# Kernel tuning notes

Hardware: AMD Instinct MI355X
Metric: run time of the kernel (lower is better)

The kernel has to match this reference:

```python
import jax, jax.numpy as jnp
import numpy as np

NUM_HEADS = 8

def _gelu(x):
    return jax.nn.gelu(x, approximate=False)

def _ln(x, w, b, eps=1e-5):
    m = x.mean(-1, keepdims=True)
    v = ((x - m) ** 2).mean(-1, keepdims=True)
    return (x - m) / jnp.sqrt(v + eps) * w + b

def _conv(x, w, pad):
    return jax.lax.conv_general_dilated(x, w, (1, 1), [(pad, pad), (pad, pad)],
                                        dimension_numbers=('NCHW', 'OIHW', 'NCHW'))

def _dwconv(x, w):
    return jax.lax.conv_general_dilated(x, w, (1, 1), [(1, 1), (1, 1)],
                                        feature_group_count=x.shape[1],
                                        dimension_numbers=('NCHW', 'OIHW', 'NCHW'))

def setup_inputs():
    B, T, N, C, K = 4, 3, 4096, 256, 100
    ks = jax.random.split(jax.random.key(0), 16)
    p = lambda i, shape: (0.02 * jax.random.normal(ks[i], shape)).astype(jnp.float32)
    z = lambda n: jnp.zeros((n,), jnp.float32)
    return {
        'x': jax.random.normal(ks[0], (B, N, C), jnp.float32),
        'mem': jax.random.normal(ks[1], (B * T, N, C), jnp.float32),
        'conv1_w': p(2, (C, C, 7, 7)), 'conv1_b': z(C),
        'conv2_w': p(3, (C, C, 1, 1)), 'conv2_b': z(C),
        'conv3_w': p(4, (K, C, 1, 1)),
        'sim_alpha': jnp.ones((1,), jnp.float32), 'sim_beta': jnp.zeros((1,), jnp.float32),
        'ln_w': jnp.ones((C,), jnp.float32), 'ln_b': z(C),
        'q_w': p(5, (C, C)), 'q_b': z(C),
        'k_w': p(6, (C, C)), 'k_b': z(C),
        'v_w': p(7, (C, C)), 'v_b': z(C),
        'proj_w': p(8, (C, C)), 'proj_b': z(C),
        'fc1_w': p(9, (4 * C, C)), 'fc1_b': z(4 * C),
        'dw_w': p(10, (4 * C, 1, 3, 3)), 'dw_b': z(4 * C),
        'fc2_w': p(11, (C, 4 * C)), 'fc2_b': z(C),
        'H': 64, 'W': 64, 't': 3,
    }

def reference(x, mem, conv1_w, conv1_b, conv2_w, conv2_b, conv3_w, sim_alpha, sim_beta,
              ln_w, ln_b, q_w, q_b, k_w, k_b, v_w, v_b, proj_w, proj_b,
              fc1_w, fc1_b, dw_w, dw_b, fc2_w, fc2_b, H, W, t):
    B, N, C = x.shape
    T = t + 1
    # stack memory frames with current frame: [B, T, N, C]
    xt = jnp.concatenate([mem.reshape(B, t, N, C), x[:, None]], axis=1)
    img = xt.reshape(B * T, N, C).transpose(0, 2, 1).reshape(B * T, C, H, W)
    h = _gelu(_conv(img, conv1_w, 3) + conv1_b[:, None, None])
    h = _gelu(_conv(h, conv2_w, 0) + conv2_b[:, None, None])
    cz = _conv(h, conv3_w, 0)                      # [B*T, K, H, W]
    K = cz.shape[1]
    center = jax.nn.softmax(cz.reshape(B, T, K, N), axis=-1)
    center = jnp.einsum('btkn,btnc->btkc', center, xt)  # cluster centers [B,T,K,C]
    last, prev = center[:, -1], center[:, :-1]
    num = jnp.einsum('bkc,bskc->bsk', last, prev)
    den = jnp.maximum(jnp.linalg.norm(last, axis=-1)[:, None] * jnp.linalg.norm(prev, axis=-1), 1e-8)
    cos = jax.nn.sigmoid(sim_beta + sim_alpha * (num / den))  # [B, T-1, K]
    C_in = last + (cos[..., None] * prev).sum(axis=1)
    C_in = _ln(C_in, ln_w, ln_b)
    # cross-attention: queries = current frame tokens, keys/values = centers
    hd = C // NUM_HEADS
    q = (x @ q_w.T + q_b).reshape(B, N, NUM_HEADS, hd) * (hd ** -0.5)
    k = (C_in @ k_w.T + k_b).reshape(B, K, NUM_HEADS, hd)
    v = (C_in @ v_w.T + v_b).reshape(B, K, NUM_HEADS, hd)
    attn = jax.nn.softmax(jnp.einsum('bnhd,bkhd->bhnk', q, k), axis=-1)
    o = jnp.einsum('bhnk,bkhd->bnhd', attn, v).reshape(B, N, C)
    o = o @ proj_w.T + proj_b
    out = x + _ln(o, ln_w, ln_b)
    # MLP with depthwise conv
    y = out @ fc1_w.T + fc1_b                      # [B, N, 4C]
    yi = y.transpose(0, 2, 1).reshape(B, 4 * C, H, W)
    yi = _dwconv(yi, dw_w) + dw_b[:, None, None]
    y = _gelu(yi.reshape(B, 4 * C, N).transpose(0, 2, 1))
    y = y @ fc2_w.T + fc2_b
    return out + _ln(y, ln_w, ln_b)
```

## Files before the change

### kernel.cpp

```cpp
#include <hip/hip_runtime.h>
#include <math.h>

#define NN 4096
#define CC 256
#define HH 64
#define BT 16
#define KCC 100
#define NHH 8
#define HDD 32
#define C4 1024

typedef unsigned short bf16_t;
typedef short s16x8 __attribute__((ext_vector_type(8)));
typedef float f32x4 __attribute__((ext_vector_type(4)));

__device__ __forceinline__ float bf2f(bf16_t h) {
  return __uint_as_float(((unsigned)h) << 16);
}
__device__ __forceinline__ bf16_t f2bf(float f) {
  unsigned u = __float_as_uint(f);
  return (bf16_t)((u + 0x7FFFu + ((u >> 16) & 1u)) >> 16);
}

__device__ __forceinline__ float gelu_f(float x) {
  return 0.5f * x * (1.0f + erff(x * 0.7071067811865475f));
}

__device__ __forceinline__ void g2l16(const void* g, void* l) {
  __builtin_amdgcn_global_load_lds((const __attribute__((address_space(1))) void*)g,
                                   (__attribute__((address_space(3))) void*)l, 16, 0, 0);
}

__device__ __forceinline__ float block_sum256(float v) {
  __shared__ float sh[4];
#pragma unroll
  for (int off = 32; off; off >>= 1) v += __shfl_xor(v, off, 64);
  __syncthreads();
  if ((threadIdx.x & 63) == 0) sh[threadIdx.x >> 6] = v;
  __syncthreads();
  return sh[0] + sh[1] + sh[2] + sh[3];
}

__device__ __forceinline__ const float* xt_base(const float* x, const float* mem, int bt) {
  int b = bt >> 2, tt = bt & 3;
  return (tt < 3) ? (mem + (size_t)(b * 3 + tt) * NN * CC)
                  : (x + (size_t)b * NN * CC);
}

__global__ __launch_bounds__(256) void prologue(const float* __restrict__ x,
                                                const float* __restrict__ mem,
                                                bf16_t* __restrict__ xtb,
                                                const float* __restrict__ w1,
                                                bf16_t* __restrict__ wtb,
                                                const float* __restrict__ c2w,
                                                const float* __restrict__ c3w,
                                                const float* __restrict__ qw,
                                                const float* __restrict__ pw,
                                                const float* __restrict__ f1w,
                                                const float* __restrict__ f2w,
                                                bf16_t* __restrict__ wbz) {
  int bid = blockIdx.x;
  int tid = threadIdx.x;
  if (bid < 16384) {
    int i = bid * 256 + tid;
    int c4 = i & 63;
    int n = (i >> 6) & 4095;
    int bt = i >> 18;
    const float* src = xt_base(x, mem, bt) + (size_t)n * CC + c4 * 4;
    float4 v = *(const float4*)src;
    ushort4 o;
    o.x = f2bf(v.x); o.y = f2bf(v.y); o.z = f2bf(v.z); o.w = f2bf(v.w);
    *(ushort4*)(xtb + (size_t)i * 4) = o;
  } else if (bid < 19520) {
    int i = (bid - 16384) * 256 + tid;
    int cj = i & 7;
    int t = i >> 3;
    int co = t & 63; t >>= 6;
    int oc = t & 3; t >>= 2;
    int kx = t % 7; t /= 7;
    int cq = t & 3; t >>= 2;
    int cg = t & 7;
    int ky = t >> 3;
    int ci = cg * 32 + oc * 8 + cj;
    int cog = cq * 64 + co;
    wtb[i] = f2bf(w1[((size_t)(cog * CC + ci) * 7 + ky) * 7 + kx]);
  } else {
    int j = (bid - 19520) * 256 + tid;
    float v;
    if (j < 65536) v = c2w[j];
    else if (j < 91136) v = c3w[j - 65536];
    else if (j < 156672) v = qw[j - 91136];
    else if (j < 222208) v = pw[j - 156672];
    else if (j < 484352) v = f1w[j - 222208];
    else v = f2w[j - 484352];
    wbz[j] = f2bf(v);
  }
}

__global__ __launch_bounds__(256, 2) void conv1_mfma(const bf16_t* __restrict__ xtb,
                                                     const bf16_t* __restrict__ wtb,
                                                     const float* __restrict__ bias,
                                                     bf16_t* __restrict__ h1) {
  int cq = blockIdx.x >> 8;
  int bt = (blockIdx.x >> 4) & 15;
  int h0 = (blockIdx.x & 15) * 4;
  int co0 = cq * 64;
  int tid = threadIdx.x;
  int wv = tid >> 6;
  int lane = tid & 63;
  int lm = lane & 15;
  int g = lane >> 4;
  __shared__ short As[10][4][70][8];
  __shared__ short Ws[7][4][64][8];
  {
    s16x8 z = {0, 0, 0, 0, 0, 0, 0, 0};
    for (int i = tid; i < 2800; i += 256) *(s16x8*)((short*)As + i * 8) = z;
  }
  __syncthreads();
  f32x4 acc[4][4] = {};
  const bf16_t* xb = xtb + (size_t)bt * (NN * CC);
  for (int cig = 0; cig < 8; ++cig) {
    int ci0 = cig * 32;
    for (int t = wv; t < 40; t += 4) {
      int rr = t >> 2, go = t & 3;
      int r = h0 - 3 + rr;
      if (r >= 0 && r < HH) {
        const bf16_t* gsrc = xb + ((size_t)(r * 64 + lane)) * CC + ci0 + go * 8;
        g2l16(gsrc, &As[rr][go][3][0]);
      }
    }
    for (int ky = 0; ky < 7; ++ky) {
      const bf16_t* wk = wtb + ((size_t)((ky * 8 + cig) * 4 + cq)) * (1792 * 8);
      for (int t = wv; t < 28; t += 4)
        g2l16(wk + (size_t)t * 512 + lane * 8, (short*)Ws + t * 512);
      __syncthreads();
#pragma unroll
      for (int kx = 0; kx < 7; ++kx) {
        s16x8 af[4], bf[4];
#pragma unroll
        for (int mt = 0; mt < 4; ++mt)
          af[mt] = *(const s16x8*)&As[wv + ky][g][mt * 16 + lm + kx][0];
#pragma unroll
        for (int nt = 0; nt < 4; ++nt)
          bf[nt] = *(const s16x8*)&Ws[kx][g][nt * 16 + lm][0];
#pragma unroll
        for (int mt = 0; mt < 4; ++mt)
#pragma unroll
          for (int nt = 0; nt < 4; ++nt)
            acc[mt][nt] = __builtin_amdgcn_mfma_f32_16x16x32_bf16(af[mt], bf[nt],
                                                                  acc[mt][nt], 0, 0, 0);
      }
      __syncthreads();
    }
  }
  int row = h0 + wv;
  const size_t xbase = (size_t)bt * (NN * CC);
#pragma unroll
  for (int nt = 0; nt < 4; ++nt) {
    int co = co0 + nt * 16 + lm;
    float bs = bias[co];
#pragma unroll
    for (int mt = 0; mt < 4; ++mt) {
#pragma unroll
      for (int rg = 0; rg < 4; ++rg) {
        int col = mt * 16 + g * 4 + rg;
        float vv = acc[mt][nt][rg] + bs;
        h1[xbase + (size_t)(row * 64 + col) * CC + co] = f2bf(gelu_f(vv));
      }
    }
  }
}

template <int GELU, int BIAS, int TOUT, int OBF>
__global__ __launch_bounds__(256) void gemm_mfma(const bf16_t* __restrict__ A,
                                                 const bf16_t* __restrict__ W,
                                                 const float* __restrict__ bias,
                                                 void* __restrict__ outp,
                                                 int M, int N, int K, int ldo,
                                                 size_t aStr, size_t oStr) {
  __shared__ short As[128][40];
  __shared__ short Bs[128][40];
  A += (size_t)blockIdx.z * aStr;
  size_t obase = (size_t)blockIdx.z * oStr;
  int tid = threadIdx.x;
  int n0 = blockIdx.x * 128, m0 = blockIdx.y * 128;
  int lane = tid & 63, wv = tid >> 6;
  int wm = wv & 1, wn = wv >> 1;
  int lm = lane & 15, g = lane >> 4;
  f32x4 acc[4][4] = {};
  int r1 = tid >> 2, kq = tid & 3;
  int r2 = r1 + 64;
  for (int k0 = 0; k0 < K; k0 += 32) {
    *(s16x8*)&As[r1][kq * 8] = *(const s16x8*)(A + (size_t)(m0 + r1) * K + k0 + kq * 8);
    *(s16x8*)&As[r2][kq * 8] = *(const s16x8*)(A + (size_t)(m0 + r2) * K + k0 + kq * 8);
    s16x8 z = {0, 0, 0, 0, 0, 0, 0, 0};
    s16x8 b1 = z, b2 = z;
    if (n0 + r1 < N) b1 = *(const s16x8*)(W + (size_t)(n0 + r1) * K + k0 + kq * 8);
    if (n0 + r2 < N) b2 = *(const s16x8*)(W + (size_t)(n0 + r2) * K + k0 + kq * 8);
    *(s16x8*)&Bs[r1][kq * 8] = b1;
    *(s16x8*)&Bs[r2][kq * 8] = b2;
    __syncthreads();
    s16x8 af[4], bf[4];
#pragma unroll
    for (int mt = 0; mt < 4; ++mt)
      af[mt] = *(const s16x8*)&As[wm * 64 + mt * 16 + lm][g * 8];
#pragma unroll
    for (int nt = 0; nt < 4; ++nt)
      bf[nt] = *(const s16x8*)&Bs[wn * 64 + nt * 16 + lm][g * 8];
#pragma unroll
    for (int mt = 0; mt < 4; ++mt)
#pragma unroll
      for (int nt = 0; nt < 4; ++nt)
        acc[mt][nt] = __builtin_amdgcn_mfma_f32_16x16x32_bf16(af[mt], bf[nt],
                                                              acc[mt][nt], 0, 0, 0);
    __syncthreads();
  }
#pragma unroll
  for (int nt = 0; nt < 4; ++nt) {
    int n = n0 + wn * 64 + nt * 16 + lm;
    if (n >= N) continue;
    float bs = BIAS ? bias[n] : 0.f;
#pragma unroll
    for (int mt = 0; mt < 4; ++mt) {
#pragma unroll
      for (int rg = 0; rg < 4; ++rg) {
        int m = m0 + wm * 64 + mt * 16 + g * 4 + rg;
        float v = acc[mt][nt][rg] + bs;
        if (GELU) v = gelu_f(v);
        size_t idx = obase + (TOUT ? ((size_t)n * ldo + m) : ((size_t)m * ldo + n));
        if (OBF)
          ((bf16_t*)outp)[idx] = f2bf(v);
        else
          ((float*)outp)[idx] = v;
      }
    }
  }
}

__global__ __launch_bounds__(256) void gemm_kv(const float* __restrict__ cin,
                                               const float* __restrict__ kw,
                                               const float* __restrict__ kbias,
                                               const float* __restrict__ vw,
                                               const float* __restrict__ vbias,
                                               float* __restrict__ kout,
                                               float* __restrict__ vout) {
  const float* Wm = blockIdx.z ? vw : kw;
  const float* bias = blockIdx.z ? vbias : kbias;
  float* outp = blockIdx.z ? vout : kout;
  const int M = 400, N = 256, K = 256;
  __shared__ float As[16][68];
  __shared__ float Ws[16][68];
  int tid = threadIdx.x;
  int n0 = blockIdx.x * 64, m0 = blockIdx.y * 64;
  int txn = tid & 15, tym = tid >> 4;
  int mi = tid >> 2, kq = (tid & 3) * 4;
  float acc[4][4] = {};
  for (int k0 = 0; k0 < K; k0 += 16) {
    float4 av = {0, 0, 0, 0}, wvv = {0, 0, 0, 0};
    if (m0 + mi < M) av = *(const float4*)&cin[(size_t)(m0 + mi) * K + k0 + kq];
    if (n0 + mi < N) wvv = *(const float4*)&Wm[(size_t)(n0 + mi) * K + k0 + kq];
    As[kq + 0][mi] = av.x; As[kq + 1][mi] = av.y; As[kq + 2][mi] = av.z; As[kq + 3][mi] = av.w;
    Ws[kq + 0][mi] = wvv.x; Ws[kq + 1][mi] = wvv.y; Ws[kq + 2][mi] = wvv.z; Ws[kq + 3][mi] = wvv.w;
    __syncthreads();
#pragma unroll
    for (int ki = 0; ki < 16; ++ki) {
      float4 a4 = *(const float4*)&As[ki][tym * 4];
      float4 w4 = *(const float4*)&Ws[ki][txn * 4];
      float am[4] = {a4.x, a4.y, a4.z, a4.w};
      float wn[4] = {w4.x, w4.y, w4.z, w4.w};
#pragma unroll
      for (int i = 0; i < 4; ++i)
#pragma unroll
        for (int j = 0; j < 4; ++j) acc[i][j] += am[i] * wn[j];
    }
    __syncthreads();
  }
#pragma unroll
  for (int i = 0; i < 4; ++i) {
    int m = m0 + tym * 4 + i;
    if (m >= M) continue;
#pragma unroll
    for (int j = 0; j < 4; ++j) {
      int n = n0 + txn * 4 + j;
      outp[(size_t)m * 256 + n] = acc[i][j] + bias[n];
    }
  }
}

__global__ __launch_bounds__(256) void softmax_rows(bf16_t* __restrict__ p) {
  __shared__ float sh[8];
  int tid = threadIdx.x;
  bf16_t* base = p + (size_t)blockIdx.x * NN + tid * 16;
  s16x8 a = *(const s16x8*)base;
  s16x8 b = *(const s16x8*)(base + 8);
  float vals[16];
#pragma unroll
  for (int j = 0; j < 8; ++j) {
    vals[j] = bf2f((bf16_t)a[j]);
    vals[8 + j] = bf2f((bf16_t)b[j]);
  }
  float mx = -1e30f;
#pragma unroll
  for (int j = 0; j < 16; ++j) mx = fmaxf(mx, vals[j]);
#pragma unroll
  for (int off = 32; off; off >>= 1) mx = fmaxf(mx, __shfl_xor(mx, off, 64));
  if ((tid & 63) == 0) sh[tid >> 6] = mx;
  __syncthreads();
  mx = fmaxf(fmaxf(sh[0], sh[1]), fmaxf(sh[2], sh[3]));
  float s = 0.f;
#pragma unroll
  for (int j = 0; j < 16; ++j) {
    vals[j] = expf(vals[j] - mx);
    s += vals[j];
  }
#pragma unroll
  for (int off = 32; off; off >>= 1) s += __shfl_xor(s, off, 64);
  if ((tid & 63) == 0) sh[4 + (tid >> 6)] = s;
  __syncthreads();
  s = sh[4] + sh[5] + sh[6] + sh[7];
  float inv = 1.f / s;
  s16x8 oa, ob;
#pragma unroll
  for (int j = 0; j < 8; ++j) {
    oa[j] = (short)f2bf(vals[j] * inv);
    ob[j] = (short)f2bf(vals[8 + j] * inv);
  }
  *(s16x8*)base = oa;
  *(s16x8*)(base + 8) = ob;
}

__global__ __launch_bounds__(256) void center_mfma(const bf16_t* __restrict__ soft,
                                                   const bf16_t* __restrict__ xtb,
                                                   float* __restrict__ partial) {
  int c0 = blockIdx.x * 128;
  int bt = blockIdx.y;
  int nc = blockIdx.z;
  int tid = threadIdx.x;
  int lane = tid & 63, wv = tid >> 6;
  int wm = wv & 1, wn = wv >> 1;
  int lm = lane & 15, g = lane >> 4;
  __shared__ short As[128][40];
  __shared__ short Bs[128][40];
  f32x4 acc[4][4] = {};
  int r1 = tid >> 2, kq = tid & 3;
  int r2 = r1 + 64;
  int bk = tid & 31, bc = (tid >> 5) * 16;
  const bf16_t* sb = soft + (size_t)bt * NN + (size_t)nc * 512;
  const bf16_t* xb = xtb + ((size_t)bt * NN + (size_t)nc * 512) * CC + c0;
  for (int k0 = 0; k0 < 512; k0 += 32) {
    *(s16x8*)&As[r1][kq * 8] =
        *(const s16x8*)(sb + (size_t)r1 * (BT * NN) + k0 + kq * 8);
    if (r2 < KCC)
      *(s16x8*)&As[r2][kq * 8] =
          *(const s16x8*)(sb + (size_t)r2 * (BT * NN) + k0 + kq * 8);
    s16x8 v0 = *(const s16x8*)(xb + (size_t)(k0 + bk) * CC + bc);
    s16x8 v1 = *(const s16x8*)(xb + (size_t)(k0 + bk) * CC + bc + 8);
#pragma unroll
    for (int j = 0; j < 8; ++j) Bs[bc + j][bk] = v0[j];
#pragma unroll
    for (int j = 0; j < 8; ++j) Bs[bc + 8 + j][bk] = v1[j];
    __syncthreads();
    s16x8 af[4], bf[4];
#pragma unroll
    for (int mt = 0; mt < 4; ++mt)
      af[mt] = *(const s16x8*)&As[wm * 64 + mt * 16 + lm][g * 8];
#pragma unroll
    for (int nt = 0; nt < 4; ++nt)
      bf[nt] = *(const s16x8*)&Bs[wn * 64 + nt * 16 + lm][g * 8];
#pragma unroll
    for (int mt = 0; mt < 4; ++mt)
#pragma unroll
      for (int nt = 0; nt < 4; ++nt)
        acc[mt][nt] = __builtin_amdgcn_mfma_f32_16x16x32_bf16(af[mt], bf[nt],
                                                              acc[mt][nt], 0, 0, 0);
    __syncthreads();
  }
  size_t obase = ((size_t)nc * BT + bt) * (KCC * CC);
#pragma unroll
  for (int nt = 0; nt < 4; ++nt) {
    int c = c0 + wn * 64 + nt * 16 + lm;
#pragma unroll
    for (int mt = 0; mt < 4; ++mt) {
#pragma unroll
      for (int rg = 0; rg < 4; ++rg) {
        int m = wm * 64 + mt * 16 + g * 4 + rg;
        if (m < KCC) partial[obase + (size_t)m * CC + c] = acc[mt][nt][rg];
      }
    }
  }
}

__global__ __launch_bounds__(256) void sim_cin(const float* __restrict__ partial,
                                               const float* __restrict__ alpha_p,
                                               const float* __restrict__ beta_p,
                                               const float* __restrict__ lnw,
                                               const float* __restrict__ lnb,
                                               float* __restrict__ cin) {
  int b = blockIdx.x / KCC, kc = blockIdx.x % KCC;
  int c = threadIdx.x;
  float p0 = 0.f, p1 = 0.f, p2 = 0.f, lst = 0.f;
#pragma unroll
  for (int nc = 0; nc < 8; ++nc) {
    size_t base = ((size_t)nc * BT) * KCC * CC;
    p0 += partial[base + ((size_t)(b * 4 + 0) * KCC + kc) * CC + c];
    p1 += partial[base + ((size_t)(b * 4 + 1) * KCC + kc) * CC + c];
    p2 += partial[base + ((size_t)(b * 4 + 2) * KCC + kc) * CC + c];
    lst += partial[base + ((size_t)(b * 4 + 3) * KCC + kc) * CC + c];
  }
  float ll = block_sum256(lst * lst);
  float q0 = block_sum256(p0 * p0);
  float q1 = block_sum256(p1 * p1);
  float q2 = block_sum256(p2 * p2);
  float d0 = block_sum256(lst * p0);
  float d1 = block_sum256(lst * p1);
  float d2 = block_sum256(lst * p2);
  float alpha = alpha_p[0], beta = beta_p[0];
  float nl = sqrtf(ll);
  float c0 = 1.f / (1.f + expf(-(beta + alpha * (d0 / fmaxf(nl * sqrtf(q0), 1e-8f)))));
  float c1 = 1.f / (1.f + expf(-(beta + alpha * (d1 / fmaxf(nl * sqrtf(q1), 1e-8f)))));
  float c2 = 1.f / (1.f + expf(-(beta + alpha * (d2 / fmaxf(nl * sqrtf(q2), 1e-8f)))));
  float v = lst + c0 * p0 + c1 * p1 + c2 * p2;
  float m = block_sum256(v) * (1.f / CC);
  float dv = v - m;
  float var = block_sum256(dv * dv) * (1.f / CC);
  cin[((size_t)b * KCC + kc) * CC + c] = dv * rsqrtf(var + 1e-5f) * lnw[c] + lnb[c];
}

__global__ __launch_bounds__(256) void attn2(const float* __restrict__ q,
                                             const float* __restrict__ kb,
                                             const float* __restrict__ vb,
                                             bf16_t* __restrict__ ob) {
  int b = blockIdx.y;
  int n0 = blockIdx.x * 8;
  int tid = threadIdx.x;
  __shared__ float qs[8][256];
  __shared__ float Ks[32][257];
  __shared__ float sc[8][8][104];
#pragma unroll
  for (int r = 0; r < 8; ++r)
    qs[r][tid] = q[((size_t)b * NN + n0 + r) * CC + tid] * 0.17677669529663687f;
  int nn = tid >> 5, kcl = tid & 31;
  for (int kt = 0; kt < 4; ++kt) {
    int kbase = kt * 32;
    int rows = (kbase + 32 <= KCC) ? 32 : (KCC - kbase);
    __syncthreads();
    for (int idx = tid; idx < rows * 256; idx += 256) {
      int rr = idx >> 8, cc = idx & 255;
      Ks[rr][cc] = kb[((size_t)b * KCC + kbase + rr) * CC + cc];
    }
    __syncthreads();
    if (kcl < rows) {
#pragma unroll
      for (int h = 0; h < NHH; ++h) {
        float s = 0.f;
#pragma unroll
        for (int d = 0; d < HDD; ++d) s += qs[nn][h * HDD + d] * Ks[kcl][h * HDD + d];
        sc[nn][h][kbase + kcl] = s;
      }
    }
  }
  __syncthreads();
  {
    int tnn = tid >> 5, th = (tid >> 2) & 7, j = tid & 3;
    float mx = -1e30f;
    for (int kc = j * 25; kc < j * 25 + 25; ++kc) mx = fmaxf(mx, sc[tnn][th][kc]);
    mx = fmaxf(mx, __shfl_xor(mx, 1, 64));
    mx = fmaxf(mx, __shfl_xor(mx, 2, 64));
    float sm = 0.f;
    for (int kc = j * 25; kc < j * 25 + 25; ++kc) {
      float e = expf(sc[tnn][th][kc] - mx);
      sc[tnn][th][kc] = e;
      sm += e;
    }
    sm += __shfl_xor(sm, 1, 64);
    sm += __shfl_xor(sm, 2, 64);
    float inv = 1.f / sm;
    for (int kc = j * 25; kc < j * 25 + 25; ++kc) sc[tnn][th][kc] *= inv;
  }
  __syncthreads();
  float o[8] = {0, 0, 0, 0, 0, 0, 0, 0};
  int h = tid >> 5;
  for (int kc = 0; kc < KCC; ++kc) {
    float v = vb[((size_t)b * KCC + kc) * CC + tid];
#pragma unroll
    for (int r = 0; r < 8; ++r) o[r] += sc[r][h][kc] * v;
  }
#pragma unroll
  for (int r = 0; r < 8; ++r)
    ob[((size_t)b * NN + n0 + r) * CC + tid] = f2bf(o[r]);
}

template <int WB>
__global__ __launch_bounds__(256) void add_ln(const float* __restrict__ res,
                                              const float* __restrict__ y,
                                              const float* __restrict__ lnw,
                                              const float* __restrict__ lnb,
                                              float* __restrict__ dst,
                                              bf16_t* __restrict__ dst_b) {
  size_t row = blockIdx.x;
  int c = threadIdx.x;
  float v = y[row * CC + c];
  float m = block_sum256(v) * (1.f / CC);
  float dv = v - m;
  float var = block_sum256(dv * dv) * (1.f / CC);
  float o = res[row * CC + c] + dv * rsqrtf(var + 1e-5f) * lnw[c] + lnb[c];
  dst[row * CC + c] = o;
  if (WB) dst_b[row * CC + c] = f2bf(o);
}

__global__ __launch_bounds__(256) void dwconv_kernel(const bf16_t* __restrict__ y1,
                                                     const float* __restrict__ dww,
                                                     const float* __restrict__ dwb,
                                                     bf16_t* __restrict__ y2) {
  int b = blockIdx.x >> 12;
  int n = blockIdx.x & 4095;
  int h = n >> 6, w = n & 63;
  int c40 = threadIdx.x * 4;
  float wreg[4][9];
#pragma unroll
  for (int j = 0; j < 4; ++j)
#pragma unroll
    for (int t2 = 0; t2 < 9; ++t2) wreg[j][t2] = dww[(size_t)(c40 + j) * 9 + t2];
  float acc[4] = {0, 0, 0, 0};
#pragma unroll
  for (int dy = 0; dy < 3; ++dy) {
    int r = h + dy - 1;
    if (r < 0 || r >= HH) continue;
#pragma unroll
    for (int dx = 0; dx < 3; ++dx) {
      int cl = w + dx - 1;
      if (cl < 0 || cl >= 64) continue;
      ushort4 u = *(const ushort4*)(y1 + ((size_t)b * NN + r * 64 + cl) * C4 + c40);
      int t2 = dy * 3 + dx;
      acc[0] += bf2f(u.x) * wreg[0][t2];
      acc[1] += bf2f(u.y) * wreg[1][t2];
      acc[2] += bf2f(u.z) * wreg[2][t2];
      acc[3] += bf2f(u.w) * wreg[3][t2];
    }
  }
  ushort4 o;
  o.x = f2bf(gelu_f(acc[0] + dwb[c40 + 0]));
  o.y = f2bf(gelu_f(acc[1] + dwb[c40 + 1]));
  o.z = f2bf(gelu_f(acc[2] + dwb[c40 + 2]));
  o.w = f2bf(gelu_f(acc[3] + dwb[c40 + 3]));
  *(ushort4*)(y2 + ((size_t)b * NN + n) * C4 + c40) = o;
}

extern "C" void kernel_launch(void* const* d_in, const int* in_sizes, int n_in,
                              void* d_out, int out_size, void* d_ws, size_t ws_size,
                              hipStream_t stream) {
  const float* x = (const float*)d_in[0];
  const float* mem = (const float*)d_in[1];
  const float* conv1_w = (const float*)d_in[2];
  const float* conv1_b = (const float*)d_in[3];
  const float* conv2_w = (const float*)d_in[4];
  const float* conv2_b = (const float*)d_in[5];
  const float* conv3_w = (const float*)d_in[6];
  const float* sim_a = (const float*)d_in[7];
  const float* sim_b = (const float*)d_in[8];
  const float* ln_w = (const float*)d_in[9];
  const float* ln_b = (const float*)d_in[10];
  const float* q_w = (const float*)d_in[11];
  const float* q_b = (const float*)d_in[12];
  const float* k_w = (const float*)d_in[13];
  const float* k_b = (const float*)d_in[14];
  const float* v_w = (const float*)d_in[15];
  const float* v_b = (const float*)d_in[16];
  const float* proj_w = (const float*)d_in[17];
  const float* proj_b = (const float*)d_in[18];
  const float* fc1_w = (const float*)d_in[19];
  const float* fc1_b = (const float*)d_in[20];
  const float* dw_w = (const float*)d_in[21];
  const float* dw_b = (const float*)d_in[22];
  const float* fc2_w = (const float*)d_in[23];
  const float* fc2_b = (const float*)d_in[24];

  char* base = (char*)d_ws;
  bf16_t* xtb = (bf16_t*)(base);
  bf16_t* by1 = (bf16_t*)(base);
  bf16_t* bh1 = (bf16_t*)(base + 33554432);
  float* qb = (float*)(base + 33554432);
  float* outb = (float*)(base + 33554432);
  float* partial = (float*)(base + 50331648);
  float* pbuf = (float*)(base + 50331648);
  bf16_t* y2 = (bf16_t*)(base + 50331648);
  bf16_t* czt = (bf16_t*)(base + 67108864);
  bf16_t* obz = (bf16_t*)(base + 67108864);
  bf16_t* outb_b = (bf16_t*)(base + 67108864);
  bf16_t* wtb = (bf16_t*)(base + 80216064);
  bf16_t* h2c = (bf16_t*)(base + 80216064);
  bf16_t* wbz = (bf16_t*)(base + 96993280);
  float* cin = (float*)(base + 100124672);
  float* kb = (float*)(base + 100534272);
  float* vb = (float*)(base + 100943872);
  float* dout = (float*)d_out;

  bf16_t* conv2_wb = wbz;
  bf16_t* conv3_wb = wbz + 65536;
  bf16_t* q_wb = wbz + 91136;
  bf16_t* proj_wb = wbz + 156672;
  bf16_t* fc1_wb = wbz + 222208;
  bf16_t* fc2_wb = wbz + 484352;

  prologue<<<22436, 256, 0, stream>>>(x, mem, xtb, conv1_w, wtb, conv2_w, conv3_w,
                                      q_w, proj_w, fc1_w, fc2_w, wbz);
  conv1_mfma<<<1024, 256, 0, stream>>>(xtb, wtb, conv1_b, bh1);
  for (int i = 0; i < 2; ++i) {
    gemm_mfma<1, 1, 0, 1><<<dim3(2, 256, 1), 256, 0, stream>>>(
        bh1 + (size_t)i * 32768 * CC, conv2_wb, conv2_b, h2c, 32768, 256, 256, 256, 0, 0);
    gemm_mfma<0, 0, 1, 1><<<dim3(1, 256, 1), 256, 0, stream>>>(
        h2c, conv3_wb, nullptr, czt + (size_t)i * 32768, 32768, 100, 256, 65536, 0, 0);
  }
  softmax_rows<<<1600, 256, 0, stream>>>(czt);
  center_mfma<<<dim3(2, 16, 8), 256, 0, stream>>>(czt, xtb, partial);
  sim_cin<<<400, 256, 0, stream>>>(partial, sim_a, sim_b, ln_w, ln_b, cin);
  gemm_mfma<0, 1, 0, 0><<<dim3(2, 32, 4), 256, 0, stream>>>(
      xtb + (size_t)3 * NN * CC, q_wb, q_b, qb, 4096, 256, 256, 256,
      (size_t)4 * NN * CC, (size_t)NN * CC);
  gemm_kv<<<dim3(4, 7, 2), 256, 0, stream>>>(cin, k_w, k_b, v_w, v_b, kb, vb);
  attn2<<<dim3(512, 4), 256, 0, stream>>>(qb, kb, vb, obz);
  gemm_mfma<0, 1, 0, 0><<<dim3(2, 128, 1), 256, 0, stream>>>(obz, proj_wb, proj_b, pbuf,
                                                             16384, 256, 256, 256, 0, 0);
  add_ln<1><<<16384, 256, 0, stream>>>(x, pbuf, ln_w, ln_b, outb, outb_b);
  gemm_mfma<0, 1, 0, 1><<<dim3(8, 128, 1), 256, 0, stream>>>(outb_b, fc1_wb, fc1_b, by1,
                                                             16384, 1024, 256, 1024, 0, 0);
  dwconv_kernel<<<16384, 256, 0, stream>>>(by1, dw_w, dw_b, y2);
  gemm_mfma<0, 1, 0, 0><<<dim3(2, 32, 4), 256, 0, stream>>>(
      y2, fc2_wb, fc2_b, dout, 4096, 256, 1024, 256,
      (size_t)NN * C4, (size_t)NN * CC);
  add_ln<0><<<16384, 256, 0, stream>>>(outb, dout, ln_w, ln_b, dout, nullptr);
}
```

Measured before the change: 895.8 us.

## Enlarge conv1 tile to 16 rows and double-buffer weight loads

The 7x7 conv kernel now processes 16 output rows per block with 512 threads (8 waves, each computing 2 rows) instead of 4 rows with 256 threads. The input halo overhead per block shrinks and each weight tile is reused across more pixels. Weight tiles are double-buffered so the next ky slice loads while the current one is consumed, removing one barrier per step. The cost is twice the accumulator registers per thread, much larger LDS use, and only 256 blocks, which can hurt occupancy and GPU fill.

Result: faster. 868.0 us (-3.1%).

```diff
diff --git a/kernel.cpp b/kernel.cpp
--- a/kernel.cpp
+++ b/kernel.cpp
@@ -97,54 +97,65 @@
   }
 }
 
-__global__ __launch_bounds__(256, 2) void conv1_mfma(const bf16_t* __restrict__ xtb,
+__global__ __launch_bounds__(512, 2) void conv1_mfma(const bf16_t* __restrict__ xtb,
                                                      const bf16_t* __restrict__ wtb,
                                                      const float* __restrict__ bias,
                                                      bf16_t* __restrict__ h1) {
-  int cq = blockIdx.x >> 8;
-  int bt = (blockIdx.x >> 4) & 15;
-  int h0 = (blockIdx.x & 15) * 4;
+  int bid = blockIdx.x;
+  int cq = bid & 3;
+  int rem = bid >> 2;
+  int bt = rem & 15;
+  int rb = rem >> 4;
+  int r0 = rb * 16;
   int co0 = cq * 64;
   int tid = threadIdx.x;
   int wv = tid >> 6;
   int lane = tid & 63;
   int lm = lane & 15;
   int g = lane >> 4;
-  __shared__ short As[10][4][70][8];
-  __shared__ short Ws[7][4][64][8];
+  __shared__ __align__(16) short As[22][4][70][8];
+  __shared__ __align__(16) short Ws[2][7][4][64][8];
   {
     s16x8 z = {0, 0, 0, 0, 0, 0, 0, 0};
-    for (int i = tid; i < 2800; i += 256) *(s16x8*)((short*)As + i * 8) = z;
+    for (int i = tid; i < 22 * 4 * 70; i += 512) *(s16x8*)((short*)As + i * 8) = z;
   }
   __syncthreads();
-  f32x4 acc[4][4] = {};
+  f32x4 acc[8][4] = {};
   const bf16_t* xb = xtb + (size_t)bt * (NN * CC);
   for (int cig = 0; cig < 8; ++cig) {
     int ci0 = cig * 32;
-    for (int t = wv; t < 40; t += 4) {
+    for (int t = wv; t < 88; t += 8) {
       int rr = t >> 2, go = t & 3;
-      int r = h0 - 3 + rr;
+      int r = r0 - 3 + rr;
       if (r >= 0 && r < HH) {
         const bf16_t* gsrc = xb + ((size_t)(r * 64 + lane)) * CC + ci0 + go * 8;
         g2l16(gsrc, &As[rr][go][3][0]);
       }
     }
+    {
+      const bf16_t* wk = wtb + ((size_t)((0 * 8 + cig) * 4 + cq)) * (1792 * 8);
+      for (int t = wv; t < 28; t += 8)
+        g2l16(wk + (size_t)t * 512 + lane * 8, (short*)Ws[0] + t * 512);
+    }
+    __syncthreads();
     for (int ky = 0; ky < 7; ++ky) {
-      const bf16_t* wk = wtb + ((size_t)((ky * 8 + cig) * 4 + cq)) * (1792 * 8);
-      for (int t = wv; t < 28; t += 4)
-        g2l16(wk + (size_t)t * 512 + lane * 8, (short*)Ws + t * 512);
-      __syncthreads();
+      int cur = ky & 1;
+      if (ky < 6) {
+        const bf16_t* wk = wtb + ((size_t)(((ky + 1) * 8 + cig) * 4 + cq)) * (1792 * 8);
+        for (int t = wv; t < 28; t += 8)
+          g2l16(wk + (size_t)t * 512 + lane * 8, (short*)Ws[cur ^ 1] + t * 512);
+      }
 #pragma unroll
       for (int kx = 0; kx < 7; ++kx) {
-        s16x8 af[4], bf[4];
-#pragma unroll
-        for (int mt = 0; mt < 4; ++mt)
-          af[mt] = *(const s16x8*)&As[wv + ky][g][mt * 16 + lm + kx][0];
+        s16x8 af[8], bf[4];
+#pragma unroll
+        for (int mt = 0; mt < 8; ++mt)
+          af[mt] = *(const s16x8*)&As[2 * wv + (mt >> 2) + ky][g][(mt & 3) * 16 + lm + kx][0];
 #pragma unroll
         for (int nt = 0; nt < 4; ++nt)
-          bf[nt] = *(const s16x8*)&Ws[kx][g][nt * 16 + lm][0];
-#pragma unroll
-        for (int mt = 0; mt < 4; ++mt)
+          bf[nt] = *(const s16x8*)&Ws[cur][kx][g][nt * 16 + lm][0];
+#pragma unroll
+        for (int mt = 0; mt < 8; ++mt)
 #pragma unroll
           for (int nt = 0; nt < 4; ++nt)
             acc[mt][nt] = __builtin_amdgcn_mfma_f32_16x16x32_bf16(af[mt], bf[nt],
@@ -153,19 +164,19 @@
       __syncthreads();
     }
   }
-  int row = h0 + wv;
   const size_t xbase = (size_t)bt * (NN * CC);
 #pragma unroll
   for (int nt = 0; nt < 4; ++nt) {
     int co = co0 + nt * 16 + lm;
     float bs = bias[co];
 #pragma unroll
-    for (int mt = 0; mt < 4; ++mt) {
+    for (int mt = 0; mt < 8; ++mt) {
+      int row = r0 + 2 * wv + (mt >> 2);
+      int pxb = (mt & 3) * 16 + g * 4;
 #pragma unroll
       for (int rg = 0; rg < 4; ++rg) {
-        int col = mt * 16 + g * 4 + rg;
         float vv = acc[mt][nt][rg] + bs;
-        h1[xbase + (size_t)(row * 64 + col) * CC + co] = f2bf(gelu_f(vv));
+        h1[xbase + (size_t)(row * 64 + pxb + rg) * CC + co] = f2bf(gelu_f(vv));
       }
     }
   }
@@ -604,7 +615,7 @@
 
   prologue<<<22436, 256, 0, stream>>>(x, mem, xtb, conv1_w, wtb, conv2_w, conv3_w,
                                       q_w, proj_w, fc1_w, fc2_w, wbz);
-  conv1_mfma<<<1024, 256, 0, stream>>>(xtb, wtb, conv1_b, bh1);
+  conv1_mfma<<<256, 512, 0, stream>>>(xtb, wtb, conv1_b, bh1);
   for (int i = 0; i < 2; ++i) {
     gemm_mfma<1, 1, 0, 1><<<dim3(2, 256, 1), 256, 0, stream>>>(
         bh1 + (size_t)i * 32768 * CC, conv2_wb, conv2_b, h2c, 32768, 256, 256, 256, 0, 0);
```
